# Kernel tuning notes

Measured on AMD Instinct MI355X. Metric: run time of the kernel, lower is better.

The kernel has to match this reference:

```python
import jax, jax.numpy as jnp
import numpy as np

B, H = 1024, 1024
V_OUT, V_INP = 50000, 32000
SRC = 256


def setup_inputs() -> dict:
    key = jax.random.key(0)
    ks = jax.random.split(key, 8)
    x = jax.random.normal(ks[0], (B, H), dtype=jnp.float32)
    W = jax.random.normal(ks[1], (V_OUT, H), dtype=jnp.float32) * 0.02
    b = jax.random.normal(ks[2], (V_OUT,), dtype=jnp.float32) * 0.02
    attn_scores = jax.random.uniform(ks[3], (B, SRC), dtype=jnp.float32)
    ctx_ids = jax.random.randint(ks[4], (B, SRC), 0, V_INP)
    inp_to_act = jax.random.randint(ks[5], (V_INP,), 0, V_OUT)
    out_map = jax.random.randint(ks[6], (V_OUT,), 0, V_OUT)
    actionmask = jax.random.randint(ks[7], (B, V_OUT), 0, 2).astype(jnp.int32)
    return {"x": x, "W": W, "b": b, "attn_scores": attn_scores,
            "ctx_ids": ctx_ids, "inp_to_act": inp_to_act,
            "out_map": out_map, "actionmask": actionmask}


def reference(x, W, b, attn_scores, ctx_ids, inp_to_act, out_map, actionmask):
    # gen scores: dense projection to output vocab, then remap rare ids
    gen_scores = x @ W.T + b                      # [B, V_out]
    gen_scores = gen_scores[:, out_map]           # index_select along vocab

    # pointer distribution: scatter-add attention mass onto input vocab ids
    bsz = gen_scores.shape[0]
    inpdist = jnp.zeros((bsz, V_INP), dtype=gen_scores.dtype)
    inpdist = inpdist.at[jnp.arange(bsz)[:, None], ctx_ids].add(attn_scores)

    # map input-vocab mass onto output vocab ids (scatter/set)
    ptr_scores = jnp.zeros((bsz, V_OUT), dtype=gen_scores.dtype)
    ptr_scores = ptr_scores.at[:, inp_to_act].set(inpdist)

    out_scores = gen_scores + ptr_scores
    gen_masked = gen_scores + (-1e6) * actionmask.astype(gen_scores.dtype)
    out_probs = jax.nn.softmax(out_scores, axis=-1)
    return (out_probs, gen_masked)
```

## Files before the change

kernel.cpp:

```cpp
#include <hip/hip_runtime.h>
#include <hip/hip_bf16.h>

#define B_    1024
#define H_    1024
#define VOUT  50000
#define VINP  32000
#define SRC_  256

#define BM 128
#define BN 128
#define BKK 32
#define LDK 40

typedef __bf16 bf16x8 __attribute__((ext_vector_type(8)));
typedef __bf16 bf16x4 __attribute__((ext_vector_type(4)));
typedef float  f32x4  __attribute__((ext_vector_type(4)));

__global__ void init_src_kernel(int* __restrict__ src_inp) {
    int i = blockIdx.x * blockDim.x + threadIdx.x;
    if (i < VOUT) src_inp[i] = -1;
}

__global__ void scat_max_kernel(const int* __restrict__ i2a, int* __restrict__ src_inp) {
    int v = blockIdx.x * blockDim.x + threadIdx.x;
    if (v < VINP) atomicMax(&src_inp[i2a[v]], v);
}

__global__ __launch_bounds__(256) void gemm_kernel(
    const float* __restrict__ x, const float* __restrict__ W,
    const float* __restrict__ bias, const int* __restrict__ out_map,
    const int* __restrict__ amask,
    float* __restrict__ out_scores, float* __restrict__ gen_masked)
{
    __shared__ __bf16 As[BM * LDK];
    __shared__ __bf16 Bs[BN * LDK];

    const int t  = threadIdx.x;
    const int m0 = blockIdx.x * BM;
    const int n0 = blockIdx.y * BN;

    const int tr = t >> 3;
    const int tk = (t & 7) << 2;

    const float* xrow[4];
    const float* wrow[4];
    #pragma unroll
    for (int p = 0; p < 4; ++p) {
        int r = tr + p * 32;
        xrow[p] = x + (size_t)(m0 + r) * H_ + tk;
        int n = n0 + r; if (n >= VOUT) n = VOUT - 1;
        int om = out_map[n];
        wrow[p] = W + (size_t)om * H_ + tk;
    }

    f32x4 acc[4][4];
    #pragma unroll
    for (int i = 0; i < 4; ++i)
        #pragma unroll
        for (int j = 0; j < 4; ++j)
            acc[i][j] = (f32x4){0.f, 0.f, 0.f, 0.f};

    const int wv   = t >> 6;
    const int wm   = (wv >> 1) * 64;
    const int wn   = (wv & 1) * 64;
    const int lane = t & 63;
    const int quad = lane >> 4;
    const int lr   = lane & 15;

    for (int k0 = 0; k0 < H_; k0 += BKK) {
        #pragma unroll
        for (int p = 0; p < 4; ++p) {
            int r = tr + p * 32;
            const float4 av = *(const float4*)(xrow[p] + k0);
            const float4 bv = *(const float4*)(wrow[p] + k0);
            bf16x4 a4, b4;
            a4.x = (__bf16)av.x; a4.y = (__bf16)av.y; a4.z = (__bf16)av.z; a4.w = (__bf16)av.w;
            b4.x = (__bf16)bv.x; b4.y = (__bf16)bv.y; b4.z = (__bf16)bv.z; b4.w = (__bf16)bv.w;
            *(bf16x4*)(&As[r * LDK + tk]) = a4;
            *(bf16x4*)(&Bs[r * LDK + tk]) = b4;
        }
        __syncthreads();

        bf16x8 af[4], bfr[4];
        #pragma unroll
        for (int i = 0; i < 4; ++i) {
            af[i]  = *(const bf16x8*)(&As[(wm + i * 16 + lr) * LDK + quad * 8]);
            bfr[i] = *(const bf16x8*)(&Bs[(wn + i * 16 + lr) * LDK + quad * 8]);
        }
        #pragma unroll
        for (int mi = 0; mi < 4; ++mi)
            #pragma unroll
            for (int ni = 0; ni < 4; ++ni)
                acc[mi][ni] = __builtin_amdgcn_mfma_f32_16x16x32_bf16(af[mi], bfr[ni], acc[mi][ni], 0, 0, 0);
        __syncthreads();
    }

    #pragma unroll
    for (int ni = 0; ni < 4; ++ni) {
        int n = n0 + wn + ni * 16 + lr;
        if (n >= VOUT) continue;
        float bb = bias[out_map[n]];
        #pragma unroll
        for (int mi = 0; mi < 4; ++mi) {
            int mbase = m0 + wm + mi * 16 + quad * 4;
            #pragma unroll
            for (int r = 0; r < 4; ++r) {
                size_t off = (size_t)(mbase + r) * VOUT + n;
                float v = acc[mi][ni][r] + bb;
                out_scores[off] = v;
                gen_masked[off] = v - 1000000.0f * (float)amask[off];
            }
        }
    }
}

__global__ void ptr_scatter_kernel(const float* __restrict__ attn,
                                   const int* __restrict__ ctx,
                                   const int* __restrict__ i2a,
                                   const int* __restrict__ src_inp,
                                   float* __restrict__ out_scores)
{
    int idx = blockIdx.x * blockDim.x + threadIdx.x;
    int i = idx >> 8;
    int v = ctx[idx];
    int o = i2a[v];
    if (src_inp[o] == v)
        atomicAdd(out_scores + (size_t)i * VOUT + o, attn[idx]);
}

__global__ __launch_bounds__(256) void softmax_kernel(float* __restrict__ probs)
{
    const int row = blockIdx.x;
    float* p = probs + (size_t)row * VOUT;
    float4* p4 = (float4*)p;
    const int N4 = VOUT / 4;
    const int t = threadIdx.x;
    __shared__ float red[256];

    float m = -1e30f;
    for (int i = t; i < N4; i += 256) {
        float4 v = p4[i];
        m = fmaxf(m, fmaxf(fmaxf(v.x, v.y), fmaxf(v.z, v.w)));
    }
    red[t] = m; __syncthreads();
    for (int s = 128; s > 0; s >>= 1) {
        if (t < s) red[t] = fmaxf(red[t], red[t + s]);
        __syncthreads();
    }
    m = red[0]; __syncthreads();

    float sum = 0.f;
    for (int i = t; i < N4; i += 256) {
        float4 v = p4[i];
        sum += __expf(v.x - m) + __expf(v.y - m) + __expf(v.z - m) + __expf(v.w - m);
    }
    red[t] = sum; __syncthreads();
    for (int s = 128; s > 0; s >>= 1) {
        if (t < s) red[t] += red[t + s];
        __syncthreads();
    }
    float inv = 1.0f / red[0];
    __syncthreads();

    for (int i = t; i < N4; i += 256) {
        float4 v = p4[i];
        v.x = __expf(v.x - m) * inv;
        v.y = __expf(v.y - m) * inv;
        v.z = __expf(v.z - m) * inv;
        v.w = __expf(v.w - m) * inv;
        p4[i] = v;
    }
}

extern "C" void kernel_launch(void* const* d_in, const int* in_sizes, int n_in,
                              void* d_out, int out_size, void* d_ws, size_t ws_size,
                              hipStream_t stream)
{
    const float* x     = (const float*)d_in[0];
    const float* W     = (const float*)d_in[1];
    const float* b     = (const float*)d_in[2];
    const float* attn  = (const float*)d_in[3];
    const int*   ctx   = (const int*)d_in[4];
    const int*   i2a   = (const int*)d_in[5];
    const int*   omap  = (const int*)d_in[6];
    const int*   amask = (const int*)d_in[7];

    float* out_probs  = (float*)d_out;
    float* gen_masked = out_probs + (size_t)B_ * VOUT;

    int* src_inp = (int*)d_ws;

    init_src_kernel<<<(VOUT + 255) / 256, 256, 0, stream>>>(src_inp);
    scat_max_kernel<<<(VINP + 255) / 256, 256, 0, stream>>>(i2a, src_inp);

    dim3 grid(B_ / BM, (VOUT + BN - 1) / BN);
    gemm_kernel<<<grid, 256, 0, stream>>>(x, W, b, omap, amask, out_probs, gen_masked);

    ptr_scatter_kernel<<<(B_ * SRC_) / 256, 256, 0, stream>>>(attn, ctx, i2a, src_inp, out_probs);

    softmax_kernel<<<B_, 256, 0, stream>>>(out_probs);
}
```

Measured before the change: 1.162 ms.

## Fuse softmax row sums into GEMM epilogue and drop max pass

The GEMM epilogue now writes float4-vectorized outputs with swapped MFMA operands so each lane owns four contiguous columns, and it accumulates per-row exp sums into a global rowsum through atomics. The pointer scatter corrects that sum with exp(new)-exp(old). A light normalization kernel replaces the three-pass softmax. The change also adds register prefetch of the next K tile, a swizzled block order for L2 reuse, and removes the LDS padding. Because the max subtraction is gone, exp could overflow if the logits were large. Removing the LDS padding may also bring back bank conflicts.

```diff
diff --git a/kernel.cpp b/kernel.cpp
--- a/kernel.cpp
+++ b/kernel.cpp
@@ -10,15 +10,17 @@
 #define BM 128
 #define BN 128
 #define BKK 32
-#define LDK 40
 
 typedef __bf16 bf16x8 __attribute__((ext_vector_type(8)));
 typedef __bf16 bf16x4 __attribute__((ext_vector_type(4)));
 typedef float  f32x4  __attribute__((ext_vector_type(4)));
 
-__global__ void init_src_kernel(int* __restrict__ src_inp) {
+__global__ void init_kernel(int* __restrict__ src_inp,
+                            float* __restrict__ rowsum)
+{
     int i = blockIdx.x * blockDim.x + threadIdx.x;
     if (i < VOUT) src_inp[i] = -1;
+    if (i < B_)  rowsum[i] = 0.0f;
 }
 
 __global__ void scat_max_kernel(const int* __restrict__ i2a, int* __restrict__ src_inp) {
@@ -30,15 +32,21 @@
     const float* __restrict__ x, const float* __restrict__ W,
     const float* __restrict__ bias, const int* __restrict__ out_map,
     const int* __restrict__ amask,
-    float* __restrict__ out_scores, float* __restrict__ gen_masked)
-{
-    __shared__ __bf16 As[BM * LDK];
-    __shared__ __bf16 Bs[BN * LDK];
+    float* __restrict__ out_scores, float* __restrict__ gen_masked,
+    float* __restrict__ rowsum)
+{
+    __shared__ __bf16 As[BM * BKK];
+    __shared__ __bf16 Bs[BN * BKK];
+
+    const int id = (int)(blockIdx.x + (blockIdx.y << 3));
+    const int g  = id >> 3;
+    const int by = (id & 7) * 49 + (g >> 3);
+    if (by >= 391) return;
+    const int bx = g & 7;
+    const int m0 = bx * BM;
+    const int n0 = by * BN;
 
     const int t  = threadIdx.x;
-    const int m0 = blockIdx.x * BM;
-    const int n0 = blockIdx.y * BN;
-
     const int tr = t >> 3;
     const int tk = (t & 7) << 2;
 
@@ -49,8 +57,7 @@
         int r = tr + p * 32;
         xrow[p] = x + (size_t)(m0 + r) * H_ + tk;
         int n = n0 + r; if (n >= VOUT) n = VOUT - 1;
-        int om = out_map[n];
-        wrow[p] = W + (size_t)om * H_ + tk;
+        wrow[p] = W + (size_t)out_map[n] * H_ + tk;
     }
 
     f32x4 acc[4][4];
@@ -67,50 +74,75 @@
     const int quad = lane >> 4;
     const int lr   = lane & 15;
 
+    float4 ar[4], br[4];
+    #pragma unroll
+    for (int p = 0; p < 4; ++p) {
+        ar[p] = *(const float4*)(xrow[p]);
+        br[p] = *(const float4*)(wrow[p]);
+    }
+
     for (int k0 = 0; k0 < H_; k0 += BKK) {
         #pragma unroll
         for (int p = 0; p < 4; ++p) {
             int r = tr + p * 32;
-            const float4 av = *(const float4*)(xrow[p] + k0);
-            const float4 bv = *(const float4*)(wrow[p] + k0);
             bf16x4 a4, b4;
-            a4.x = (__bf16)av.x; a4.y = (__bf16)av.y; a4.z = (__bf16)av.z; a4.w = (__bf16)av.w;
-            b4.x = (__bf16)bv.x; b4.y = (__bf16)bv.y; b4.z = (__bf16)bv.z; b4.w = (__bf16)bv.w;
-            *(bf16x4*)(&As[r * LDK + tk]) = a4;
-            *(bf16x4*)(&Bs[r * LDK + tk]) = b4;
+            a4.x = (__bf16)ar[p].x; a4.y = (__bf16)ar[p].y; a4.z = (__bf16)ar[p].z; a4.w = (__bf16)ar[p].w;
+            b4.x = (__bf16)br[p].x; b4.y = (__bf16)br[p].y; b4.z = (__bf16)br[p].z; b4.w = (__bf16)br[p].w;
+            *(bf16x4*)(&As[r * BKK + tk]) = a4;
+            *(bf16x4*)(&Bs[r * BKK + tk]) = b4;
         }
         __syncthreads();
 
+        if (k0 + BKK < H_) {
+            #pragma unroll
+            for (int p = 0; p < 4; ++p) {
+                ar[p] = *(const float4*)(xrow[p] + k0 + BKK);
+                br[p] = *(const float4*)(wrow[p] + k0 + BKK);
+            }
+        }
+
         bf16x8 af[4], bfr[4];
         #pragma unroll
         for (int i = 0; i < 4; ++i) {
-            af[i]  = *(const bf16x8*)(&As[(wm + i * 16 + lr) * LDK + quad * 8]);
-            bfr[i] = *(const bf16x8*)(&Bs[(wn + i * 16 + lr) * LDK + quad * 8]);
+            af[i]  = *(const bf16x8*)(&As[(wm + i * 16 + lr) * BKK + quad * 8]);
+            bfr[i] = *(const bf16x8*)(&Bs[(wn + i * 16 + lr) * BKK + quad * 8]);
         }
         #pragma unroll
         for (int mi = 0; mi < 4; ++mi)
             #pragma unroll
             for (int ni = 0; ni < 4; ++ni)
-                acc[mi][ni] = __builtin_amdgcn_mfma_f32_16x16x32_bf16(af[mi], bfr[ni], acc[mi][ni], 0, 0, 0);
+                acc[mi][ni] = __builtin_amdgcn_mfma_f32_16x16x32_bf16(bfr[ni], af[mi], acc[mi][ni], 0, 0, 0);
         __syncthreads();
     }
 
     #pragma unroll
-    for (int ni = 0; ni < 4; ++ni) {
-        int n = n0 + wn + ni * 16 + lr;
-        if (n >= VOUT) continue;
-        float bb = bias[out_map[n]];
-        #pragma unroll
-        for (int mi = 0; mi < 4; ++mi) {
-            int mbase = m0 + wm + mi * 16 + quad * 4;
-            #pragma unroll
-            for (int r = 0; r < 4; ++r) {
-                size_t off = (size_t)(mbase + r) * VOUT + n;
-                float v = acc[mi][ni][r] + bb;
-                out_scores[off] = v;
-                gen_masked[off] = v - 1000000.0f * (float)amask[off];
+    for (int mi = 0; mi < 4; ++mi) {
+        const int m = m0 + wm + mi * 16 + lr;
+        float psum = 0.0f;
+        #pragma unroll
+        for (int ni = 0; ni < 4; ++ni) {
+            const int n = n0 + wn + ni * 16 + (quad << 2);
+            if (n < VOUT) {
+                const size_t off = (size_t)m * VOUT + n;
+                float4 v;
+                v.x = acc[mi][ni][0] + bias[out_map[n + 0]];
+                v.y = acc[mi][ni][1] + bias[out_map[n + 1]];
+                v.z = acc[mi][ni][2] + bias[out_map[n + 2]];
+                v.w = acc[mi][ni][3] + bias[out_map[n + 3]];
+                *(float4*)(out_scores + off) = v;
+                const int4 am = *(const int4*)(amask + off);
+                float4 gm;
+                gm.x = v.x - 1000000.0f * (float)am.x;
+                gm.y = v.y - 1000000.0f * (float)am.y;
+                gm.z = v.z - 1000000.0f * (float)am.z;
+                gm.w = v.w - 1000000.0f * (float)am.w;
+                *(float4*)(gen_masked + off) = gm;
+                psum += __expf(v.x) + __expf(v.y) + __expf(v.z) + __expf(v.w);
             }
         }
+        psum += __shfl_xor(psum, 16, 64);
+        psum += __shfl_xor(psum, 32, 64);
+        if (quad == 0) atomicAdd(rowsum + m, psum);
     }
 }
 
@@ -118,56 +150,33 @@
                                    const int* __restrict__ ctx,
                                    const int* __restrict__ i2a,
                                    const int* __restrict__ src_inp,
-                                   float* __restrict__ out_scores)
+                                   float* __restrict__ out_scores,
+                                   float* __restrict__ rowsum)
 {
     int idx = blockIdx.x * blockDim.x + threadIdx.x;
     int i = idx >> 8;
     int v = ctx[idx];
     int o = i2a[v];
-    if (src_inp[o] == v)
-        atomicAdd(out_scores + (size_t)i * VOUT + o, attn[idx]);
-}
-
-__global__ __launch_bounds__(256) void softmax_kernel(float* __restrict__ probs)
+    if (src_inp[o] == v) {
+        float a   = attn[idx];
+        float old = atomicAdd(out_scores + (size_t)i * VOUT + o, a);
+        atomicAdd(rowsum + i, __expf(old + a) - __expf(old));
+    }
+}
+
+__global__ __launch_bounds__(256) void norm_kernel(float* __restrict__ probs,
+                                                   const float* __restrict__ rowsum)
 {
     const int row = blockIdx.x;
-    float* p = probs + (size_t)row * VOUT;
-    float4* p4 = (float4*)p;
-    const int N4 = VOUT / 4;
-    const int t = threadIdx.x;
-    __shared__ float red[256];
-
-    float m = -1e30f;
-    for (int i = t; i < N4; i += 256) {
+    const float inv = 1.0f / rowsum[row];
+    float4* p4 = (float4*)(probs + (size_t)row * VOUT);
+    const int base = blockIdx.y * 3125;
+    for (int i = base + threadIdx.x; i < base + 3125; i += 256) {
         float4 v = p4[i];
-        m = fmaxf(m, fmaxf(fmaxf(v.x, v.y), fmaxf(v.z, v.w)));
-    }
-    red[t] = m; __syncthreads();
-    for (int s = 128; s > 0; s >>= 1) {
-        if (t < s) red[t] = fmaxf(red[t], red[t + s]);
-        __syncthreads();
-    }
-    m = red[0]; __syncthreads();
-
-    float sum = 0.f;
-    for (int i = t; i < N4; i += 256) {
-        float4 v = p4[i];
-        sum += __expf(v.x - m) + __expf(v.y - m) + __expf(v.z - m) + __expf(v.w - m);
-    }
-    red[t] = sum; __syncthreads();
-    for (int s = 128; s > 0; s >>= 1) {
-        if (t < s) red[t] += red[t + s];
-        __syncthreads();
-    }
-    float inv = 1.0f / red[0];
-    __syncthreads();
-
-    for (int i = t; i < N4; i += 256) {
-        float4 v = p4[i];
-        v.x = __expf(v.x - m) * inv;
-        v.y = __expf(v.y - m) * inv;
-        v.z = __expf(v.z - m) * inv;
-        v.w = __expf(v.w - m) * inv;
+        v.x = __expf(v.x) * inv;
+        v.y = __expf(v.y) * inv;
+        v.z = __expf(v.z) * inv;
+        v.w = __expf(v.w) * inv;
         p4[i] = v;
     }
 }
@@ -188,15 +197,18 @@
     float* out_probs  = (float*)d_out;
     float* gen_masked = out_probs + (size_t)B_ * VOUT;
 
-    int* src_inp = (int*)d_ws;
-
-    init_src_kernel<<<(VOUT + 255) / 256, 256, 0, stream>>>(src_inp);
+    int*   src_inp = (int*)d_ws;
+    float* rowsum  = (float*)(src_inp + VOUT);
+
+    init_kernel<<<(VOUT + 255) / 256, 256, 0, stream>>>(src_inp, rowsum);
     scat_max_kernel<<<(VINP + 255) / 256, 256, 0, stream>>>(i2a, src_inp);
 
-    dim3 grid(B_ / BM, (VOUT + BN - 1) / BN);
-    gemm_kernel<<<grid, 256, 0, stream>>>(x, W, b, omap, amask, out_probs, gen_masked);
-
-    ptr_scatter_kernel<<<(B_ * SRC_) / 256, 256, 0, stream>>>(attn, ctx, i2a, src_inp, out_probs);
-
-    softmax_kernel<<<B_, 256, 0, stream>>>(out_probs);
-}
+    dim3 grid(B_ / BM, 392);
+    gemm_kernel<<<grid, 256, 0, stream>>>(x, W, b, omap, amask,
+                                          out_probs, gen_masked, rowsum);
+
+    ptr_scatter_kernel<<<(B_ * SRC_) / 256, 256, 0, stream>>>(attn, ctx, i2a, src_inp,
+                                                              out_probs, rowsum);
+
+    norm_kernel<<<dim3(B_, 4), 256, 0, stream>>>(out_probs, rowsum);
+}
```

After: 1.170 ms. About the same (+0.7%).
